# Kernel optimization log

Hardware: AMD Instinct MI355X
Metric: run time of the kernel (lower is better)

## Reference

```python
import jax, jax.numpy as jnp
import numpy as np

N_USER, N_SUB, H, E, L, F_MOVIE = 500_000, 50_000, 128, 600_000, 200_000, 1250


def setup_inputs() -> dict:
    key = jax.random.key(0)
    ks = jax.random.split(key, 24)

    def p(k, shape, scale):
        return jax.random.normal(k, shape, dtype=jnp.float32) * scale

    inp = {
        "user_node_id": jnp.arange(N_USER, dtype=jnp.int32),
        "subreddit_node_id": jnp.arange(N_SUB, dtype=jnp.int32),
        "subreddit_x": jax.random.normal(ks[0], (N_SUB, F_MOVIE), dtype=jnp.float32),
        "edge_index": jnp.stack([
            jax.random.randint(ks[1], (E,), 0, N_USER, dtype=jnp.int32),
            jax.random.randint(ks[2], (E,), 0, N_SUB, dtype=jnp.int32),
        ]),
        "edge_label_index": jnp.stack([
            jax.random.randint(ks[3], (L,), 0, N_USER, dtype=jnp.int32),
            jax.random.randint(ks[4], (L,), 0, N_SUB, dtype=jnp.int32),
        ]),
        "user_emb": p(ks[5], (N_USER, H), 1.0),
        "movie_emb": p(ks[6], (N_SUB, H), 1.0),
        "movie_lin_w": p(ks[7], (F_MOVIE, H), 0.02),
        "movie_lin_b": jnp.zeros((H,), jnp.float32),
    }
    # 4 SAGEConvs: (layer1|layer2) x (user->subreddit | subreddit->user)
    for i, name in enumerate(["l1_u2s", "l1_s2u", "l2_u2s", "l2_s2u"]):
        inp[name + "_wl"] = p(ks[8 + 2 * i], (H, H), 0.05)  # lin_l: on aggregated neighbors
        inp[name + "_bl"] = jnp.zeros((H,), jnp.float32)
        inp[name + "_wr"] = p(ks[9 + 2 * i], (H, H), 0.05)  # lin_r: on root/dst features
    return inp


def _sage(x_src, x_dst, src, dst, n_dst, wl, bl, wr):
    # PyG SAGEConv(aggr='mean'): lin_l(mean_j x_src[j]) + lin_r(x_dst)
    msg = x_src[src]  # [E, H] gather
    agg = jax.ops.segment_sum(msg, dst, num_segments=n_dst)  # [n_dst, H] scatter-add
    cnt = jax.ops.segment_sum(jnp.ones((src.shape[0],), msg.dtype), dst, num_segments=n_dst)
    mean = agg / jnp.maximum(cnt, 1.0)[:, None]  # isolated dst nodes -> 0
    return mean @ wl + bl + x_dst @ wr


def reference(user_node_id, subreddit_node_id, subreddit_x, edge_index, edge_label_index,
              user_emb, movie_emb, movie_lin_w, movie_lin_b,
              l1_u2s_wl, l1_u2s_bl, l1_u2s_wr, l1_s2u_wl, l1_s2u_bl, l1_s2u_wr,
              l2_u2s_wl, l2_u2s_bl, l2_u2s_wr, l2_s2u_wl, l2_s2u_bl, l2_s2u_wr):
    src_u, dst_s = edge_index[0], edge_index[1]
    x_u = user_emb[user_node_id]  # [N_USER, H]
    x_s = subreddit_x @ movie_lin_w + movie_lin_b + movie_emb[subreddit_node_id]  # [N_SUB, H]

    # layer 1 (to_hetero: one SAGEConv per edge type, relu per node type)
    h_s = jax.nn.relu(_sage(x_u, x_s, src_u, dst_s, x_s.shape[0], l1_u2s_wl, l1_u2s_bl, l1_u2s_wr))
    h_u = jax.nn.relu(_sage(x_s, x_u, dst_s, src_u, x_u.shape[0], l1_s2u_wl, l1_s2u_bl, l1_s2u_wr))

    # layer 2 (no activation)
    o_s = _sage(h_u, h_s, src_u, dst_s, h_s.shape[0], l2_u2s_wl, l2_u2s_bl, l2_u2s_wr)
    o_u = _sage(h_s, h_u, dst_s, src_u, h_u.shape[0], l2_s2u_wl, l2_s2u_bl, l2_s2u_wr)

    # classifier: gather + dot product per supervision edge -> [L]
    return (o_u[edge_label_index[0]] * o_s[edge_label_index[1]]).sum(axis=-1)
```

## Files before the change

### kernel.cpp

```cpp
#include <hip/hip_runtime.h>

#define H 128

__global__ void deg_kernel(const int* __restrict__ src, const int* __restrict__ dst,
                           float* __restrict__ deg_u, float* __restrict__ deg_s, int E) {
    int e = blockIdx.x * blockDim.x + threadIdx.x;
    if (e < E) {
        atomicAdd(deg_u + src[e], 1.0f);
        atomicAdd(deg_s + dst[e], 1.0f);
    }
}

__global__ void scatter_kernel(const float* __restrict__ x, const int* __restrict__ src_idx,
                               const int* __restrict__ dst_idx, float* agg, int E) {
    int e = blockIdx.x * 2 + (threadIdx.x >> 7);
    int c = threadIdx.x & 127;
    if (e < E) {
        int s = src_idx[e];
        int d = dst_idx[e];
        atomicAdd(agg + (size_t)d * H + c, x[(size_t)s * H + c]);
    }
}

__global__ __launch_bounds__(256) void xs_kernel(
        const float* __restrict__ X,
        const float* __restrict__ W,
        const float* __restrict__ b,
        const float* __restrict__ emb,
        float* __restrict__ out, int n, int F) {
    __shared__ float At[32][68];
    __shared__ float Wt[32][H];

    int t = threadIdx.x;
    int row0 = blockIdx.x * 64;
    int tx = t & 31, ty = t >> 5;
    int c0 = tx * 4, r0 = ty * 8;

    float acc[8][4];
#pragma unroll
    for (int i = 0; i < 8; ++i)
#pragma unroll
        for (int j = 0; j < 4; ++j) acc[i][j] = 0.f;

    int sr = t >> 2;
    int sk = (t & 3) * 8;
    int grow = row0 + sr; if (grow > n - 1) grow = n - 1;
    const float* xrow = X + (size_t)grow * F;

    int nkb = (F + 31) / 32;
    for (int kb = 0; kb < nkb; ++kb) {
        int kbase = kb * 32;
        __syncthreads();
#pragma unroll
        for (int j = 0; j < 8; ++j) {
            int kk = kbase + sk + j;
            At[sk + j][sr] = (kk < F) ? xrow[kk] : 0.f;
        }
        const float4* wp = (const float4*)(W + (size_t)kbase * H);
        float4* wt = (float4*)&Wt[0][0];
#pragma unroll
        for (int j = 0; j < 4; ++j) {
            int f = t + j * 256;
            int k = f >> 5;
            float4 v = make_float4(0.f, 0.f, 0.f, 0.f);
            if (kbase + k < F) v = wp[f];
            wt[f] = v;
        }
        __syncthreads();
#pragma unroll
        for (int k = 0; k < 32; ++k) {
            float4 w4 = *(const float4*)&Wt[k][c0];
            float4 a0 = *(const float4*)&At[k][r0];
            float4 a1 = *(const float4*)&At[k][r0 + 4];
            float a[8] = {a0.x, a0.y, a0.z, a0.w, a1.x, a1.y, a1.z, a1.w};
            float w[4] = {w4.x, w4.y, w4.z, w4.w};
#pragma unroll
            for (int i = 0; i < 8; ++i)
#pragma unroll
                for (int j = 0; j < 4; ++j) acc[i][j] += a[i] * w[j];
        }
    }

    float4 bias = *(const float4*)(b + c0);
#pragma unroll
    for (int i = 0; i < 8; ++i) {
        int gr = row0 + r0 + i;
        if (gr < n) {
            float4 em = *(const float4*)(emb + (size_t)gr * H + c0);
            float4 o;
            o.x = acc[i][0] + bias.x + em.x;
            o.y = acc[i][1] + bias.y + em.y;
            o.z = acc[i][2] + bias.z + em.z;
            o.w = acc[i][3] + bias.w + em.w;
            *(float4*)(out + (size_t)gr * H + c0) = o;
        }
    }
}

template <bool RELU>
__global__ __launch_bounds__(256) void combine_kernel(
        const float* agg, const float* __restrict__ deg,
        const float* __restrict__ xdst,
        const float* __restrict__ wl, const float* __restrict__ bl,
        const float* __restrict__ wr,
        float* out, int n) {
    __shared__ float At[32][68];
    __shared__ float Wt[32][H];
    __shared__ float rdeg_s[64];

    int t = threadIdx.x;
    int row0 = blockIdx.x * 64;
    if (t < 64) {
        int r = row0 + t;
        float d = (r < n) ? deg[r] : 1.0f;
        rdeg_s[t] = 1.0f / fmaxf(d, 1.0f);
    }
    int tx = t & 31, ty = t >> 5;
    int c0 = tx * 4, r0 = ty * 8;

    float acc[8][4];
#pragma unroll
    for (int i = 0; i < 8; ++i)
#pragma unroll
        for (int j = 0; j < 4; ++j) acc[i][j] = 0.f;

    int sr = t >> 2;
    int sk = (t & 3) * 8;
    int grow = row0 + sr; if (grow > n - 1) grow = n - 1;

    for (int kb = 0; kb < 8; ++kb) {
        const float* src = (kb < 4) ? agg : xdst;
        const float* W   = (kb < 4) ? wl : wr;
        int kbase = (kb & 3) * 32;
        __syncthreads();
        float scale = (kb < 4) ? rdeg_s[sr] : 1.0f;
        const float* p = src + (size_t)grow * H + kbase + sk;
        float4 v0 = *(const float4*)p;
        float4 v1 = *(const float4*)(p + 4);
        At[sk + 0][sr] = v0.x * scale;
        At[sk + 1][sr] = v0.y * scale;
        At[sk + 2][sr] = v0.z * scale;
        At[sk + 3][sr] = v0.w * scale;
        At[sk + 4][sr] = v1.x * scale;
        At[sk + 5][sr] = v1.y * scale;
        At[sk + 6][sr] = v1.z * scale;
        At[sk + 7][sr] = v1.w * scale;
        const float4* wp = (const float4*)(W + (size_t)kbase * H);
        float4* wt = (float4*)&Wt[0][0];
#pragma unroll
        for (int j = 0; j < 4; ++j) {
            int f = t + j * 256;
            wt[f] = wp[f];
        }
        __syncthreads();
#pragma unroll
        for (int k = 0; k < 32; ++k) {
            float4 w4 = *(const float4*)&Wt[k][c0];
            float4 a0 = *(const float4*)&At[k][r0];
            float4 a1 = *(const float4*)&At[k][r0 + 4];
            float a[8] = {a0.x, a0.y, a0.z, a0.w, a1.x, a1.y, a1.z, a1.w};
            float w[4] = {w4.x, w4.y, w4.z, w4.w};
#pragma unroll
            for (int i = 0; i < 8; ++i)
#pragma unroll
                for (int j = 0; j < 4; ++j) acc[i][j] += a[i] * w[j];
        }
    }

    float4 bias = *(const float4*)(bl + c0);
#pragma unroll
    for (int i = 0; i < 8; ++i) {
        int gr = row0 + r0 + i;
        if (gr < n) {
            float4 o;
            o.x = acc[i][0] + bias.x;
            o.y = acc[i][1] + bias.y;
            o.z = acc[i][2] + bias.z;
            o.w = acc[i][3] + bias.w;
            if (RELU) {
                o.x = fmaxf(o.x, 0.f);
                o.y = fmaxf(o.y, 0.f);
                o.z = fmaxf(o.z, 0.f);
                o.w = fmaxf(o.w, 0.f);
            }
            *(float4*)(out + (size_t)gr * H + c0) = o;
        }
    }
}

__global__ void classifier_kernel(const float* __restrict__ o_u, const float* __restrict__ o_s,
                                  const int* __restrict__ li_u, const int* __restrict__ li_s,
                                  float* __restrict__ out, int L) {
    int wave = (int)((blockIdx.x * (size_t)blockDim.x + threadIdx.x) >> 6);
    int lane = threadIdx.x & 63;
    if (wave >= L) return;
    int a = li_u[wave];
    int b = li_s[wave];
    const float* pu = o_u + (size_t)a * H;
    const float* ps = o_s + (size_t)b * H;
    float v = pu[lane] * ps[lane] + pu[lane + 64] * ps[lane + 64];
#pragma unroll
    for (int off = 32; off > 0; off >>= 1) v += __shfl_xor(v, off);
    if (lane == 0) out[wave] = v;
}

extern "C" void kernel_launch(void* const* d_in, const int* in_sizes, int n_in,
                              void* d_out, int out_size, void* d_ws, size_t ws_size,
                              hipStream_t stream) {
    const float* sub_x     = (const float*)d_in[2];
    const int*   ei        = (const int*)d_in[3];
    const int*   eli       = (const int*)d_in[4];
    const float* user_emb  = (const float*)d_in[5];
    const float* movie_emb = (const float*)d_in[6];
    const float* mlw       = (const float*)d_in[7];
    const float* mlb       = (const float*)d_in[8];
    const float* w[4][3];
    for (int i = 0; i < 4; ++i) {
        w[i][0] = (const float*)d_in[9 + 3 * i];
        w[i][1] = (const float*)d_in[10 + 3 * i];
        w[i][2] = (const float*)d_in[11 + 3 * i];
    }

    int N_u = in_sizes[5] / H;
    int N_s = in_sizes[6] / H;
    int F   = in_sizes[7] / H;
    int E   = in_sizes[3] / 2;
    int L   = in_sizes[4] / 2;

    const int* src_u = ei;
    const int* dst_s = ei + E;
    const int* lu = eli;
    const int* ls = eli + L;

    float* x_s   = (float*)d_ws;
    float* agg_s = x_s + (size_t)N_s * H;
    float* h_s   = agg_s + (size_t)N_s * H;
    float* agg_u = h_s + (size_t)N_s * H;
    float* h_u   = agg_u + (size_t)N_u * H;
    float* deg_u = h_u + (size_t)N_u * H;
    float* deg_s = deg_u + N_u;

    size_t subBytes = (size_t)N_s * H * sizeof(float);
    size_t usrBytes = (size_t)N_u * H * sizeof(float);

    hipMemsetAsync(agg_s, 0, subBytes, stream);
    hipMemsetAsync(agg_u, 0, usrBytes, stream);
    hipMemsetAsync(deg_u, 0, (size_t)N_u * sizeof(float), stream);
    hipMemsetAsync(deg_s, 0, (size_t)N_s * sizeof(float), stream);

    deg_kernel<<<(E + 255) / 256, 256, 0, stream>>>(src_u, dst_s, deg_u, deg_s, E);
    xs_kernel<<<(N_s + 63) / 64, 256, 0, stream>>>(sub_x, mlw, mlb, movie_emb, x_s, N_s, F);

    scatter_kernel<<<(E + 1) / 2, 256, 0, stream>>>(user_emb, src_u, dst_s, agg_s, E);
    combine_kernel<true><<<(N_s + 63) / 64, 256, 0, stream>>>(
        agg_s, deg_s, x_s, w[0][0], w[0][1], w[0][2], h_s, N_s);
    scatter_kernel<<<(E + 1) / 2, 256, 0, stream>>>(x_s, dst_s, src_u, agg_u, E);
    combine_kernel<true><<<(N_u + 63) / 64, 256, 0, stream>>>(
        agg_u, deg_u, user_emb, w[1][0], w[1][1], w[1][2], h_u, N_u);

    hipMemsetAsync(agg_s, 0, subBytes, stream);
    hipMemsetAsync(agg_u, 0, usrBytes, stream);
    scatter_kernel<<<(E + 1) / 2, 256, 0, stream>>>(h_u, src_u, dst_s, agg_s, E);
    combine_kernel<false><<<(N_s + 63) / 64, 256, 0, stream>>>(
        agg_s, deg_s, h_s, w[2][0], w[2][1], w[2][2], x_s , N_s);
    scatter_kernel<<<(E + 1) / 2, 256, 0, stream>>>(h_s, dst_s, src_u, agg_u, E);
    combine_kernel<false><<<(N_u + 63) / 64, 256, 0, stream>>>(
        agg_u, deg_u, h_u, w[3][0], w[3][1], w[3][2], agg_u , N_u);

    classifier_kernel<<<(L + 3) / 4, 256, 0, stream>>>(
        agg_u, x_s, lu, ls, (float*)d_out, L);
}
```

Baseline: 2.954 ms.

## Reassociate user-side SAGE linear before scatter and fold final layer into classifier

```diff
diff --git a/kernel.cpp b/kernel.cpp
--- a/kernel.cpp
+++ b/kernel.cpp
@@ -99,11 +99,11 @@
 
 template <bool RELU>
 __global__ __launch_bounds__(256) void combine_kernel(
-        const float* agg, const float* __restrict__ deg,
+        const float* __restrict__ agg, const float* __restrict__ deg,
         const float* __restrict__ xdst,
         const float* __restrict__ wl, const float* __restrict__ bl,
         const float* __restrict__ wr,
-        float* out, int n) {
+        float* __restrict__ out, int n) {
     __shared__ float At[32][68];
     __shared__ float Wt[32][H];
     __shared__ float rdeg_s[64];
@@ -188,20 +188,192 @@
     }
 }
 
-__global__ void classifier_kernel(const float* __restrict__ o_u, const float* __restrict__ o_s,
-                                  const int* __restrict__ li_u, const int* __restrict__ li_s,
-                                  float* __restrict__ out, int L) {
-    int wave = (int)((blockIdx.x * (size_t)blockDim.x + threadIdx.x) >> 6);
+__global__ __launch_bounds__(256) void gemm_k(
+        const float* __restrict__ A, const float* __restrict__ W,
+        float* __restrict__ out, int n) {
+    __shared__ float At[32][68];
+    __shared__ float Wt[32][H];
+
+    int t = threadIdx.x;
+    int row0 = blockIdx.x * 64;
+    int tx = t & 31, ty = t >> 5;
+    int c0 = tx * 4, r0 = ty * 8;
+
+    float acc[8][4];
+#pragma unroll
+    for (int i = 0; i < 8; ++i)
+#pragma unroll
+        for (int j = 0; j < 4; ++j) acc[i][j] = 0.f;
+
+    int sr = t >> 2;
+    int sk = (t & 3) * 8;
+    int grow = row0 + sr; if (grow > n - 1) grow = n - 1;
+
+    for (int kb = 0; kb < 4; ++kb) {
+        int kbase = kb * 32;
+        __syncthreads();
+        const float* p = A + (size_t)grow * H + kbase + sk;
+        float4 v0 = *(const float4*)p;
+        float4 v1 = *(const float4*)(p + 4);
+        At[sk + 0][sr] = v0.x;
+        At[sk + 1][sr] = v0.y;
+        At[sk + 2][sr] = v0.z;
+        At[sk + 3][sr] = v0.w;
+        At[sk + 4][sr] = v1.x;
+        At[sk + 5][sr] = v1.y;
+        At[sk + 6][sr] = v1.z;
+        At[sk + 7][sr] = v1.w;
+        const float4* wp = (const float4*)(W + (size_t)kbase * H);
+        float4* wt = (float4*)&Wt[0][0];
+#pragma unroll
+        for (int j = 0; j < 4; ++j) {
+            int f = t + j * 256;
+            wt[f] = wp[f];
+        }
+        __syncthreads();
+#pragma unroll
+        for (int k = 0; k < 32; ++k) {
+            float4 w4 = *(const float4*)&Wt[k][c0];
+            float4 a0 = *(const float4*)&At[k][r0];
+            float4 a1 = *(const float4*)&At[k][r0 + 4];
+            float a[8] = {a0.x, a0.y, a0.z, a0.w, a1.x, a1.y, a1.z, a1.w};
+            float w[4] = {w4.x, w4.y, w4.z, w4.w};
+#pragma unroll
+            for (int i = 0; i < 8; ++i)
+#pragma unroll
+                for (int j = 0; j < 4; ++j) acc[i][j] += a[i] * w[j];
+        }
+    }
+
+#pragma unroll
+    for (int i = 0; i < 8; ++i) {
+        int gr = row0 + r0 + i;
+        if (gr < n) {
+            float4 o = make_float4(acc[i][0], acc[i][1], acc[i][2], acc[i][3]);
+            *(float4*)(out + (size_t)gr * H + c0) = o;
+        }
+    }
+}
+
+template <bool RELU>
+__global__ __launch_bounds__(256) void ucombine_kernel(
+        const float* __restrict__ agg, const float* __restrict__ deg,
+        const float* __restrict__ X,
+        const float* __restrict__ W, const float* __restrict__ b,
+        float* __restrict__ out, int n) {
+    __shared__ float At[32][68];
+    __shared__ float Wt[32][H];
+    __shared__ float rdeg_s[64];
+
+    int t = threadIdx.x;
+    int row0 = blockIdx.x * 64;
+    if (t < 64) {
+        int r = row0 + t;
+        float d = (r < n) ? deg[r] : 1.0f;
+        rdeg_s[t] = 1.0f / fmaxf(d, 1.0f);
+    }
+    int tx = t & 31, ty = t >> 5;
+    int c0 = tx * 4, r0 = ty * 8;
+
+    float acc[8][4];
+#pragma unroll
+    for (int i = 0; i < 8; ++i)
+#pragma unroll
+        for (int j = 0; j < 4; ++j) acc[i][j] = 0.f;
+
+    int sr = t >> 2;
+    int sk = (t & 3) * 8;
+    int grow = row0 + sr; if (grow > n - 1) grow = n - 1;
+
+    for (int kb = 0; kb < 4; ++kb) {
+        int kbase = kb * 32;
+        __syncthreads();
+        const float* p = X + (size_t)grow * H + kbase + sk;
+        float4 v0 = *(const float4*)p;
+        float4 v1 = *(const float4*)(p + 4);
+        At[sk + 0][sr] = v0.x;
+        At[sk + 1][sr] = v0.y;
+        At[sk + 2][sr] = v0.z;
+        At[sk + 3][sr] = v0.w;
+        At[sk + 4][sr] = v1.x;
+        At[sk + 5][sr] = v1.y;
+        At[sk + 6][sr] = v1.z;
+        At[sk + 7][sr] = v1.w;
+        const float4* wp = (const float4*)(W + (size_t)kbase * H);
+        float4* wt = (float4*)&Wt[0][0];
+#pragma unroll
+        for (int j = 0; j < 4; ++j) {
+            int f = t + j * 256;
+            wt[f] = wp[f];
+        }
+        __syncthreads();
+#pragma unroll
+        for (int k = 0; k < 32; ++k) {
+            float4 w4 = *(const float4*)&Wt[k][c0];
+            float4 a0 = *(const float4*)&At[k][r0];
+            float4 a1 = *(const float4*)&At[k][r0 + 4];
+            float a[8] = {a0.x, a0.y, a0.z, a0.w, a1.x, a1.y, a1.z, a1.w};
+            float w[4] = {w4.x, w4.y, w4.z, w4.w};
+#pragma unroll
+            for (int i = 0; i < 8; ++i)
+#pragma unroll
+                for (int j = 0; j < 4; ++j) acc[i][j] += a[i] * w[j];
+        }
+    }
+
+    float4 bias = *(const float4*)(b + c0);
+#pragma unroll
+    for (int i = 0; i < 8; ++i) {
+        int gr = row0 + r0 + i;
+        if (gr < n) {
+            float rd = rdeg_s[r0 + i];
+            float4 ag = *(const float4*)(agg + (size_t)gr * H + c0);
+            float4 o;
+            o.x = acc[i][0] + bias.x + ag.x * rd;
+            o.y = acc[i][1] + bias.y + ag.y * rd;
+            o.z = acc[i][2] + bias.z + ag.z * rd;
+            o.w = acc[i][3] + bias.w + ag.w * rd;
+            if (RELU) {
+                o.x = fmaxf(o.x, 0.f);
+                o.y = fmaxf(o.y, 0.f);
+                o.z = fmaxf(o.z, 0.f);
+                o.w = fmaxf(o.w, 0.f);
+            }
+            *(float4*)(out + (size_t)gr * H + c0) = o;
+        }
+    }
+}
+
+__global__ void transpose128(const float* __restrict__ in, float* __restrict__ outT) {
+    for (int idx = threadIdx.x; idx < H * H; idx += blockDim.x) {
+        int i = idx >> 7, j = idx & 127;
+        outT[(size_t)j * H + i] = in[idx];
+    }
+}
+
+__global__ void classifier2_kernel(
+        const float* __restrict__ agg2, const float* __restrict__ deg_u,
+        const float* __restrict__ bl2,
+        const float* __restrict__ h_u,
+        const float* __restrict__ o_s, const float* __restrict__ t_s,
+        const int* __restrict__ li_u, const int* __restrict__ li_s,
+        float* __restrict__ out, int L) {
+    int e = blockIdx.x * 4 + (threadIdx.x >> 6);
     int lane = threadIdx.x & 63;
-    if (wave >= L) return;
-    int a = li_u[wave];
-    int b = li_s[wave];
-    const float* pu = o_u + (size_t)a * H;
-    const float* ps = o_s + (size_t)b * H;
-    float v = pu[lane] * ps[lane] + pu[lane + 64] * ps[lane + 64];
+    if (e >= L) return;
+    int a = li_u[e];
+    int b = li_s[e];
+    float rd = 1.0f / fmaxf(deg_u[a], 1.0f);
+    float2 ag = ((const float2*)(agg2 + (size_t)a * H))[lane];
+    float2 bb = ((const float2*)bl2)[lane];
+    float2 os = ((const float2*)(o_s + (size_t)b * H))[lane];
+    float2 hu = ((const float2*)(h_u + (size_t)a * H))[lane];
+    float2 ts = ((const float2*)(t_s + (size_t)b * H))[lane];
+    float v = (ag.x * rd + bb.x) * os.x + (ag.y * rd + bb.y) * os.y
+            + hu.x * ts.x + hu.y * ts.y;
 #pragma unroll
     for (int off = 32; off > 0; off >>= 1) v += __shfl_xor(v, off);
-    if (lane == 0) out[wave] = v;
+    if (lane == 0) out[e] = v;
 }
 
 extern "C" void kernel_launch(void* const* d_in, const int* in_sizes, int n_in,
@@ -223,7 +395,6 @@
 
     int N_u = in_sizes[5] / H;
     int N_s = in_sizes[6] / H;
-    int F   = in_sizes[7] / H;
     int E   = in_sizes[3] / 2;
     int L   = in_sizes[4] / 2;
 
@@ -235,10 +406,13 @@
     float* x_s   = (float*)d_ws;
     float* agg_s = x_s + (size_t)N_s * H;
     float* h_s   = agg_s + (size_t)N_s * H;
-    float* agg_u = h_s + (size_t)N_s * H;
+    float* ybuf  = h_s + (size_t)N_s * H;
+    float* t_s   = ybuf + (size_t)N_s * H;
+    float* agg_u = t_s + (size_t)N_s * H;
     float* h_u   = agg_u + (size_t)N_u * H;
     float* deg_u = h_u + (size_t)N_u * H;
     float* deg_s = deg_u + N_u;
+    float* wrT   = deg_s + N_s;
 
     size_t subBytes = (size_t)N_s * H * sizeof(float);
     size_t usrBytes = (size_t)N_u * H * sizeof(float);
@@ -249,24 +423,29 @@
     hipMemsetAsync(deg_s, 0, (size_t)N_s * sizeof(float), stream);
 
     deg_kernel<<<(E + 255) / 256, 256, 0, stream>>>(src_u, dst_s, deg_u, deg_s, E);
-    xs_kernel<<<(N_s + 63) / 64, 256, 0, stream>>>(sub_x, mlw, mlb, movie_emb, x_s, N_s, F);
-
+    xs_kernel<<<(N_s + 63) / 64, 256, 0, stream>>>(sub_x, mlw, mlb, movie_emb, x_s, N_s, 1250);
+
+    int gs = (N_s + 63) / 64;
+    int gu = (N_u + 63) / 64;
+
+    gemm_k<<<gs, 256, 0, stream>>>(x_s, w[1][0], ybuf, N_s);
+    scatter_kernel<<<(E + 1) / 2, 256, 0, stream>>>(ybuf, dst_s, src_u, agg_u, E);
     scatter_kernel<<<(E + 1) / 2, 256, 0, stream>>>(user_emb, src_u, dst_s, agg_s, E);
-    combine_kernel<true><<<(N_s + 63) / 64, 256, 0, stream>>>(
+    combine_kernel<true><<<gs, 256, 0, stream>>>(
         agg_s, deg_s, x_s, w[0][0], w[0][1], w[0][2], h_s, N_s);
-    scatter_kernel<<<(E + 1) / 2, 256, 0, stream>>>(x_s, dst_s, src_u, agg_u, E);
-    combine_kernel<true><<<(N_u + 63) / 64, 256, 0, stream>>>(
-        agg_u, deg_u, user_emb, w[1][0], w[1][1], w[1][2], h_u, N_u);
+    ucombine_kernel<true><<<gu, 256, 0, stream>>>(
+        agg_u, deg_u, user_emb, w[1][2], w[1][1], h_u, N_u);
 
     hipMemsetAsync(agg_s, 0, subBytes, stream);
     hipMemsetAsync(agg_u, 0, usrBytes, stream);
     scatter_kernel<<<(E + 1) / 2, 256, 0, stream>>>(h_u, src_u, dst_s, agg_s, E);
-    combine_kernel<false><<<(N_s + 63) / 64, 256, 0, stream>>>(
+    combine_kernel<false><<<gs, 256, 0, stream>>>(
         agg_s, deg_s, h_s, w[2][0], w[2][1], w[2][2], x_s , N_s);
-    scatter_kernel<<<(E + 1) / 2, 256, 0, stream>>>(h_s, dst_s, src_u, agg_u, E);
-    combine_kernel<false><<<(N_u + 63) / 64, 256, 0, stream>>>(
-        agg_u, deg_u, h_u, w[3][0], w[3][1], w[3][2], agg_u , N_u);
-
-    classifier_kernel<<<(L + 3) / 4, 256, 0, stream>>>(
-        agg_u, x_s, lu, ls, (float*)d_out, L);
-}
+    gemm_k<<<gs, 256, 0, stream>>>(h_s, w[3][0], ybuf, N_s);
+    scatter_kernel<<<(E + 1) / 2, 256, 0, stream>>>(ybuf, dst_s, src_u, agg_u, E);
+    transpose128<<<1, 256, 0, stream>>>(w[3][2], wrT);
+    gemm_k<<<gs, 256, 0, stream>>>(x_s , wrT, t_s, N_s);
+
+    classifier2_kernel<<<(L + 3) / 4, 256, 0, stream>>>(
+        agg_u, deg_u, w[3][1], h_u, x_s , t_s, lu, ls, (float*)d_out, L);
+}
```

After: 2.540 ms. -14.0%, faster.
